# Performance work log

Hardware: AMD Instinct MI355X
Metric: run time of the kernel (lower is better)

Reference implementation:

```python
import jax, jax.numpy as jnp
import numpy as np

N = 50000       # nodes
E = 800000      # edges
IN = 128        # in_channels
HID = 64        # hidden_channels
OUT = 32        # out_channels
H = 4           # heads
EH = 64         # edge_hidden_channels
EOUT = 2        # edge_out_channels
NEG_SLOPE = 0.2 # PyG GATConv default


def gat_conv(x, edge_index, W, att_src, att_dst, bias, num_nodes):
    """PyG GATConv, concat=False, add_self_loops=False, eval mode (no dropout).
    edge_attr is ignored because edge_dim=None (lin_edge is None in PyG).
    Returns (out [N, C], alpha [E, H])."""
    heads, C = att_src.shape
    xl = (x @ W).reshape(-1, heads, C)                 # [N, H, C]
    src, dst = edge_index[0], edge_index[1]
    a_src = jnp.sum(xl * att_src, axis=-1)             # [N, H]
    a_dst = jnp.sum(xl * att_dst, axis=-1)             # [N, H]
    alpha = jax.nn.leaky_relu(a_src[src] + a_dst[dst], NEG_SLOPE)  # [E, H]
    # segment softmax over destination nodes
    amax = jax.ops.segment_max(alpha, dst, num_segments=num_nodes)
    amax = jnp.where(jnp.isfinite(amax), amax, 0.0)
    ex = jnp.exp(alpha - amax[dst])
    denom = jax.ops.segment_sum(ex, dst, num_segments=num_nodes)
    alpha_n = ex / (denom[dst] + 1e-16)                # [E, H]
    msg = xl[src] * alpha_n[:, :, None]                # [E, H, C]
    out = jax.ops.segment_sum(msg, dst, num_segments=num_nodes)  # [N, H, C]
    out = out.mean(axis=1) + bias                      # concat=False -> head mean
    return out, alpha_n


def setup_inputs() -> dict:
    key = jax.random.key(0)
    ks = jax.random.split(key, 16)
    x = jax.random.normal(ks[0], (N, IN), dtype=jnp.float32)
    edge_index = jax.random.randint(ks[1], (2, E), 0, N, dtype=jnp.int32)
    edge_attr = jax.random.normal(ks[2], (E, 5), dtype=jnp.float32)
    s = lambda fan: 1.0 / np.sqrt(fan)
    W1 = jax.random.normal(ks[3], (IN, H * HID), dtype=jnp.float32) * s(IN)
    att1_src = jax.random.normal(ks[4], (H, HID), dtype=jnp.float32) * s(HID)
    att1_dst = jax.random.normal(ks[5], (H, HID), dtype=jnp.float32) * s(HID)
    b1 = jnp.zeros((HID,), dtype=jnp.float32)
    W3 = jax.random.normal(ks[6], (HID, H * OUT), dtype=jnp.float32) * s(HID)
    att3_src = jax.random.normal(ks[7], (H, OUT), dtype=jnp.float32) * s(OUT)
    att3_dst = jax.random.normal(ks[8], (H, OUT), dtype=jnp.float32) * s(OUT)
    b3 = jnp.zeros((OUT,), dtype=jnp.float32)
    EIN = 2 * OUT + H  # cat(out_src, alpha, out_dst)
    mW1 = jax.random.normal(ks[9], (EIN, EH), dtype=jnp.float32) * s(EIN)
    mb1 = jnp.zeros((EH,), dtype=jnp.float32)
    mW2 = jax.random.normal(ks[10], (EH, EOUT), dtype=jnp.float32) * s(EH)
    mb2 = jnp.zeros((EOUT,), dtype=jnp.float32)
    return {"x": x, "edge_index": edge_index, "edge_attr": edge_attr,
            "return_attention_weights": 1,
            "W1": W1, "att1_src": att1_src, "att1_dst": att1_dst, "b1": b1,
            "W3": W3, "att3_src": att3_src, "att3_dst": att3_dst, "b3": b3,
            "mW1": mW1, "mb1": mb1, "mW2": mW2, "mb2": mb2}


def reference(x, edge_index, edge_attr, return_attention_weights,
              W1, att1_src, att1_dst, b1, W3, att3_src, att3_dst, b3,
              mW1, mb1, mW2, mb2):
    edge_len = edge_attr.shape[0]  # == E (no self loops added)
    out, alpha = gat_conv(x, edge_index, W1, att1_src, att1_dst, b1, N)
    out, alpha = gat_conv(out, edge_index, W3, att3_src, att3_dst, b3, N)
    # F.dropout with training=False is the identity (eval mode)
    ei = edge_index[:, :edge_len]
    al = alpha[:edge_len, :]
    out_src = out[ei[0]]                                # [E, OUT]
    out_dst = out[ei[1]]                                # [E, OUT]
    edge_feat = jnp.concatenate([out_src, al, out_dst], axis=-1)  # [E, 2*OUT+H]
    h = jax.nn.relu(edge_feat @ mW1 + mb1)
    edge_out = h @ mW2 + mb2                            # [E, EOUT]
    return (out, edge_out)
```

## Files before the change

### kernel.cpp

```cpp
#include <hip/hip_runtime.h>
#include <hip/hip_fp16.h>

constexpr int NN   = 50000;
constexpr int EE   = 800000;
constexpr int INF  = 128;
constexpr int NH   = 4;
constexpr int GR64 = (NN + 63) / 64;
constexpr int EB   = (EE + 255) / 256;
constexpr int NCH  = (NN + 255) / 256;

struct __align__(8) h4 { __half2 a, b; };

typedef short bf16x8 __attribute__((ext_vector_type(8)));
typedef float f32x4v __attribute__((ext_vector_type(4)));

__device__ __forceinline__ float elw(float a) {
    a = (a > 0.f) ? a : 0.2f * a;
    return __expf(a);
}

__device__ __forceinline__ short bf16_hi(float x) {
    return (short)(__float_as_uint(x) >> 16);
}
__device__ __forceinline__ float bf16_back(short h) {
    return __uint_as_float(((unsigned)(unsigned short)h) << 16);
}

__global__ __launch_bounds__(256) void gemm1_mfma_k(const float* __restrict__ A,
                                                    const float* __restrict__ B,
                                                    __half* __restrict__ C,
                                                    const float* __restrict__ att_s,
                                                    const float* __restrict__ att_d,
                                                    float* __restrict__ a_s,
                                                    float* __restrict__ a_d) {
    __shared__ short Ah[64][72], Al[64][72];
    __shared__ short Bh[64][72], Bl[64][72];
    const int tid  = threadIdx.x;
    const int lane = tid & 63, w = tid >> 6;
    const int row0 = blockIdx.x * 64;
    const int head = blockIdx.y;
    const int c0   = head * 64;

    const int rl = lane & 15, gq = lane >> 4;

    f32x4v acc0 = {0,0,0,0}, acc1 = {0,0,0,0}, acc2 = {0,0,0,0}, acc3 = {0,0,0,0};

    for (int ks = 0; ks < 2; ++ks) {
        {
            const int ar = tid >> 2;
            const int kb = (tid & 3) * 4;
            const int grow = row0 + ar;
            #pragma unroll
            for (int pass = 0; pass < 4; ++pass) {
                const int kl = kb + pass * 16;
                float4 v = make_float4(0.f, 0.f, 0.f, 0.f);
                if (grow < NN) v = *(const float4*)(A + (size_t)grow * 128 + ks * 64 + kl);
                short4 hi, lo;
                hi.x = bf16_hi(v.x); lo.x = bf16_hi(v.x - bf16_back(hi.x));
                hi.y = bf16_hi(v.y); lo.y = bf16_hi(v.y - bf16_back(hi.y));
                hi.z = bf16_hi(v.z); lo.z = bf16_hi(v.z - bf16_back(hi.z));
                hi.w = bf16_hi(v.w); lo.w = bf16_hi(v.w - bf16_back(hi.w));
                *(short4*)&Ah[ar][kl] = hi;
                *(short4*)&Al[ar][kl] = lo;
            }
        }
        {
            const int c  = lane;
            const int kb = w * 16;
            #pragma unroll
            for (int chunk = 0; chunk < 2; ++chunk) {
                short hi8[8], lo8[8];
                #pragma unroll
                for (int i = 0; i < 8; ++i) {
                    const int kl = kb + chunk * 8 + i;
                    const float v = B[(size_t)(ks * 64 + kl) * 256 + c0 + c];
                    hi8[i] = bf16_hi(v);
                    lo8[i] = bf16_hi(v - bf16_back(hi8[i]));
                }
                *(bf16x8*)&Bh[c][kb + chunk * 8] =
                    (bf16x8){hi8[0],hi8[1],hi8[2],hi8[3],hi8[4],hi8[5],hi8[6],hi8[7]};
                *(bf16x8*)&Bl[c][kb + chunk * 8] =
                    (bf16x8){lo8[0],lo8[1],lo8[2],lo8[3],lo8[4],lo8[5],lo8[6],lo8[7]};
            }
        }
        __syncthreads();

        bf16x8 aH0 = *(const bf16x8*)&Ah[w * 16 + rl][gq * 8];
        bf16x8 aH1 = *(const bf16x8*)&Ah[w * 16 + rl][32 + gq * 8];
        bf16x8 aL0 = *(const bf16x8*)&Al[w * 16 + rl][gq * 8];
        bf16x8 aL1 = *(const bf16x8*)&Al[w * 16 + rl][32 + gq * 8];

        #pragma unroll
        for (int cf = 0; cf < 4; ++cf) {
            const int bc = cf * 16 + rl;
            bf16x8 bH0 = *(const bf16x8*)&Bh[bc][gq * 8];
            bf16x8 bH1 = *(const bf16x8*)&Bh[bc][32 + gq * 8];
            bf16x8 bL0 = *(const bf16x8*)&Bl[bc][gq * 8];
            bf16x8 bL1 = *(const bf16x8*)&Bl[bc][32 + gq * 8];
            f32x4v t = (cf == 0) ? acc0 : (cf == 1) ? acc1 : (cf == 2) ? acc2 : acc3;
            t = __builtin_amdgcn_mfma_f32_16x16x32_bf16(aH0, bH0, t, 0, 0, 0);
            t = __builtin_amdgcn_mfma_f32_16x16x32_bf16(aL0, bH0, t, 0, 0, 0);
            t = __builtin_amdgcn_mfma_f32_16x16x32_bf16(aH0, bL0, t, 0, 0, 0);
            t = __builtin_amdgcn_mfma_f32_16x16x32_bf16(aH1, bH1, t, 0, 0, 0);
            t = __builtin_amdgcn_mfma_f32_16x16x32_bf16(aL1, bH1, t, 0, 0, 0);
            t = __builtin_amdgcn_mfma_f32_16x16x32_bf16(aH1, bL1, t, 0, 0, 0);
            if (cf == 0) acc0 = t; else if (cf == 1) acc1 = t;
            else if (cf == 2) acc2 = t; else acc3 = t;
        }
        __syncthreads();
    }

    float sS[4] = {0.f, 0.f, 0.f, 0.f};
    float sD[4] = {0.f, 0.f, 0.f, 0.f};
    #pragma unroll
    for (int cf = 0; cf < 4; ++cf) {
        const f32x4v t = (cf == 0) ? acc0 : (cf == 1) ? acc1 : (cf == 2) ? acc2 : acc3;
        const int gcol = c0 + cf * 16 + rl;
        const float atS = att_s[gcol];
        const float atD = att_d[gcol];
        #pragma unroll
        for (int r = 0; r < 4; ++r) {
            const int grow = row0 + w * 16 + gq * 4 + r;
            if (grow < NN) C[(size_t)grow * 256 + gcol] = __float2half_rn(t[r]);
            sS[r] = fmaf(t[r], atS, sS[r]);
            sD[r] = fmaf(t[r], atD, sD[r]);
        }
    }
    #pragma unroll
    for (int r = 0; r < 4; ++r) {
        #pragma unroll
        for (int msk = 1; msk < 16; msk <<= 1) {
            sS[r] += __shfl_xor(sS[r], msk, 64);
            sD[r] += __shfl_xor(sD[r], msk, 64);
        }
    }
    if (rl == 0) {
        #pragma unroll
        for (int r = 0; r < 4; ++r) {
            const int grow = row0 + w * 16 + gq * 4 + r;
            if (grow < NN) {
                a_s[grow * NH + head] = sS[r];
                a_d[grow * NH + head] = sD[r];
            }
        }
    }
}

__global__ __launch_bounds__(256) void gemm2_mfma_k(const float* __restrict__ A,
                                                    const float* __restrict__ B,
                                                    __half* __restrict__ C,
                                                    const float* __restrict__ att_s,
                                                    const float* __restrict__ att_d,
                                                    float* __restrict__ a_s,
                                                    float* __restrict__ a_d) {
    __shared__ short Ah[64][72], Al[64][72];
    __shared__ short Bh[64][72], Bl[64][72];
    const int tid  = threadIdx.x;
    const int lane = tid & 63, w = tid >> 6;
    const int row0 = blockIdx.x * 64;
    const int c0   = blockIdx.y * 64;
    const int rl = lane & 15, gq = lane >> 4;

    {
        const int ar = tid >> 2;
        const int kb = (tid & 3) * 4;
        const int grow = row0 + ar;
        #pragma unroll
        for (int pass = 0; pass < 4; ++pass) {
            const int kl = kb + pass * 16;
            float4 v = make_float4(0.f, 0.f, 0.f, 0.f);
            if (grow < NN) v = *(const float4*)(A + (size_t)grow * 64 + kl);
            short4 hi, lo;
            hi.x = bf16_hi(v.x); lo.x = bf16_hi(v.x - bf16_back(hi.x));
            hi.y = bf16_hi(v.y); lo.y = bf16_hi(v.y - bf16_back(hi.y));
            hi.z = bf16_hi(v.z); lo.z = bf16_hi(v.z - bf16_back(hi.z));
            hi.w = bf16_hi(v.w); lo.w = bf16_hi(v.w - bf16_back(hi.w));
            *(short4*)&Ah[ar][kl] = hi;
            *(short4*)&Al[ar][kl] = lo;
        }
    }
    {
        const int c  = lane;
        const int kb = w * 16;
        #pragma unroll
        for (int chunk = 0; chunk < 2; ++chunk) {
            short hi8[8], lo8[8];
            #pragma unroll
            for (int i = 0; i < 8; ++i) {
                const int kl = kb + chunk * 8 + i;
                const float v = B[(size_t)kl * 128 + c0 + c];
                hi8[i] = bf16_hi(v);
                lo8[i] = bf16_hi(v - bf16_back(hi8[i]));
            }
            *(bf16x8*)&Bh[c][kb + chunk * 8] =
                (bf16x8){hi8[0],hi8[1],hi8[2],hi8[3],hi8[4],hi8[5],hi8[6],hi8[7]};
            *(bf16x8*)&Bl[c][kb + chunk * 8] =
                (bf16x8){lo8[0],lo8[1],lo8[2],lo8[3],lo8[4],lo8[5],lo8[6],lo8[7]};
        }
    }
    __syncthreads();

    bf16x8 aH0 = *(const bf16x8*)&Ah[w * 16 + rl][gq * 8];
    bf16x8 aH1 = *(const bf16x8*)&Ah[w * 16 + rl][32 + gq * 8];
    bf16x8 aL0 = *(const bf16x8*)&Al[w * 16 + rl][gq * 8];
    bf16x8 aL1 = *(const bf16x8*)&Al[w * 16 + rl][32 + gq * 8];

    f32x4v acc0 = {0,0,0,0}, acc1 = {0,0,0,0}, acc2 = {0,0,0,0}, acc3 = {0,0,0,0};
    #pragma unroll
    for (int cf = 0; cf < 4; ++cf) {
        const int bc = cf * 16 + rl;
        bf16x8 bH0 = *(const bf16x8*)&Bh[bc][gq * 8];
        bf16x8 bH1 = *(const bf16x8*)&Bh[bc][32 + gq * 8];
        bf16x8 bL0 = *(const bf16x8*)&Bl[bc][gq * 8];
        bf16x8 bL1 = *(const bf16x8*)&Bl[bc][32 + gq * 8];
        f32x4v t = (cf == 0) ? acc0 : (cf == 1) ? acc1 : (cf == 2) ? acc2 : acc3;
        t = __builtin_amdgcn_mfma_f32_16x16x32_bf16(aH0, bH0, t, 0, 0, 0);
        t = __builtin_amdgcn_mfma_f32_16x16x32_bf16(aL0, bH0, t, 0, 0, 0);
        t = __builtin_amdgcn_mfma_f32_16x16x32_bf16(aH0, bL0, t, 0, 0, 0);
        t = __builtin_amdgcn_mfma_f32_16x16x32_bf16(aH1, bH1, t, 0, 0, 0);
        t = __builtin_amdgcn_mfma_f32_16x16x32_bf16(aL1, bH1, t, 0, 0, 0);
        t = __builtin_amdgcn_mfma_f32_16x16x32_bf16(aH1, bL1, t, 0, 0, 0);
        if (cf == 0) acc0 = t; else if (cf == 1) acc1 = t;
        else if (cf == 2) acc2 = t; else acc3 = t;
    }

    const int h0 = c0 >> 5, h1 = h0 + 1;
    float sS0[4] = {0,0,0,0}, sD0[4] = {0,0,0,0};
    float sS1[4] = {0,0,0,0}, sD1[4] = {0,0,0,0};
    #pragma unroll
    for (int cf = 0; cf < 4; ++cf) {
        const f32x4v t = (cf == 0) ? acc0 : (cf == 1) ? acc1 : (cf == 2) ? acc2 : acc3;
        const int gcol = c0 + cf * 16 + rl;
        const float atS = att_s[gcol];
        const float atD = att_d[gcol];
        #pragma unroll
        for (int r = 0; r < 4; ++r) {
            const int grow = row0 + w * 16 + gq * 4 + r;
            if (grow < NN) C[(size_t)grow * 128 + gcol] = __float2half_rn(t[r]);
            if (cf < 2) { sS0[r] = fmaf(t[r], atS, sS0[r]); sD0[r] = fmaf(t[r], atD, sD0[r]); }
            else        { sS1[r] = fmaf(t[r], atS, sS1[r]); sD1[r] = fmaf(t[r], atD, sD1[r]); }
        }
    }
    #pragma unroll
    for (int r = 0; r < 4; ++r) {
        #pragma unroll
        for (int msk = 1; msk < 16; msk <<= 1) {
            sS0[r] += __shfl_xor(sS0[r], msk, 64);
            sD0[r] += __shfl_xor(sD0[r], msk, 64);
            sS1[r] += __shfl_xor(sS1[r], msk, 64);
            sD1[r] += __shfl_xor(sD1[r], msk, 64);
        }
    }
    if (rl == 0) {
        #pragma unroll
        for (int r = 0; r < 4; ++r) {
            const int grow = row0 + w * 16 + gq * 4 + r;
            if (grow < NN) {
                a_s[grow * NH + h0] = sS0[r];
                a_d[grow * NH + h0] = sD0[r];
                a_s[grow * NH + h1] = sS1[r];
                a_d[grow * NH + h1] = sD1[r];
            }
        }
    }
}

__global__ __launch_bounds__(256) void gemmpq_mfma_k(const float* __restrict__ A,
                                                     const float* __restrict__ B,
                                                     __half* __restrict__ C) {
    __shared__ short Ah[64][40], Al[64][40];
    __shared__ short Bh[64][40], Bl[64][40];
    const int tid  = threadIdx.x;
    const int lane = tid & 63, w = tid >> 6;
    const int row0 = blockIdx.x * 64;
    const int c0   = blockIdx.y * 64;
    const int rl = lane & 15, gq = lane >> 4;

    {
        const int ar = tid >> 2;
        const int kb = (tid & 3) * 4;
        const int grow = row0 + ar;
        #pragma unroll
        for (int pass = 0; pass < 2; ++pass) {
            const int kl = kb + pass * 16;
            float4 v = make_float4(0.f, 0.f, 0.f, 0.f);
            if (grow < NN) v = *(const float4*)(A + (size_t)grow * 32 + kl);
            short4 hi, lo;
            hi.x = bf16_hi(v.x); lo.x = bf16_hi(v.x - bf16_back(hi.x));
            hi.y = bf16_hi(v.y); lo.y = bf16_hi(v.y - bf16_back(hi.y));
            hi.z = bf16_hi(v.z); lo.z = bf16_hi(v.z - bf16_back(hi.z));
            hi.w = bf16_hi(v.w); lo.w = bf16_hi(v.w - bf16_back(hi.w));
            *(short4*)&Ah[ar][kl] = hi;
            *(short4*)&Al[ar][kl] = lo;
        }
    }
    {
        const int c = lane;
        short hi8[8], lo8[8];
        #pragma unroll
        for (int i = 0; i < 8; ++i) {
            const int kl = w * 8 + i;
            const float v = B[(size_t)kl * 128 + c0 + c];
            hi8[i] = bf16_hi(v);
            lo8[i] = bf16_hi(v - bf16_back(hi8[i]));
        }
        *(bf16x8*)&Bh[c][w * 8] =
            (bf16x8){hi8[0],hi8[1],hi8[2],hi8[3],hi8[4],hi8[5],hi8[6],hi8[7]};
        *(bf16x8*)&Bl[c][w * 8] =
            (bf16x8){lo8[0],lo8[1],lo8[2],lo8[3],lo8[4],lo8[5],lo8[6],lo8[7]};
    }
    __syncthreads();

    bf16x8 aH = *(const bf16x8*)&Ah[w * 16 + rl][gq * 8];
    bf16x8 aL = *(const bf16x8*)&Al[w * 16 + rl][gq * 8];

    #pragma unroll
    for (int cf = 0; cf < 4; ++cf) {
        const int bc = cf * 16 + rl;
        bf16x8 bH = *(const bf16x8*)&Bh[bc][gq * 8];
        bf16x8 bL = *(const bf16x8*)&Bl[bc][gq * 8];
        f32x4v t = {0, 0, 0, 0};
        t = __builtin_amdgcn_mfma_f32_16x16x32_bf16(aH, bH, t, 0, 0, 0);
        t = __builtin_amdgcn_mfma_f32_16x16x32_bf16(aL, bH, t, 0, 0, 0);
        t = __builtin_amdgcn_mfma_f32_16x16x32_bf16(aH, bL, t, 0, 0, 0);
        const int gcol = c0 + cf * 16 + rl;
        #pragma unroll
        for (int r = 0; r < 4; ++r) {
            const int grow = row0 + w * 16 + gq * 4 + r;
            if (grow < NN) C[(size_t)grow * 128 + gcol] = __float2half_rn(t[r]);
        }
    }
}


__device__ __forceinline__ void softagg1_node(int n, int lane,
                                              const int* __restrict__ rowptr,
                                              const int* __restrict__ psrc,
                                              const float* __restrict__ a_s,
                                              const float* __restrict__ a_d,
                                              const __half* __restrict__ xl,
                                              const float* __restrict__ bias,
                                              float* __restrict__ out) {
    const int r0 = rowptr[n], r1 = rowptr[n + 1];
    const int hh = lane >> 4;
    const float ad = a_d[n * NH + hh];

    const h4* X = (const h4*)xl;
    float4 A0 = {0,0,0,0}, A1 = {0,0,0,0}, A2 = {0,0,0,0}, A3 = {0,0,0,0};
    float sum = 0.f;
    int j = r0;
    for (; j + 7 < r1; j += 8) {
        const int s0 = psrc[j],     s1 = psrc[j + 1], s2 = psrc[j + 2], s3 = psrc[j + 3];
        const int s4 = psrc[j + 4], s5 = psrc[j + 5], s6 = psrc[j + 6], s7 = psrc[j + 7];
        const float w0 = elw(a_s[s0 * NH + hh] + ad);
        const float w1 = elw(a_s[s1 * NH + hh] + ad);
        const float w2 = elw(a_s[s2 * NH + hh] + ad);
        const float w3 = elw(a_s[s3 * NH + hh] + ad);
        const float w4 = elw(a_s[s4 * NH + hh] + ad);
        const float w5 = elw(a_s[s5 * NH + hh] + ad);
        const float w6 = elw(a_s[s6 * NH + hh] + ad);
        const float w7 = elw(a_s[s7 * NH + hh] + ad);
        sum += ((w0 + w1) + (w2 + w3)) + ((w4 + w5) + (w6 + w7));
        const h4 v0 = X[(size_t)s0 * 64 + lane];
        const h4 v1 = X[(size_t)s1 * 64 + lane];
        const h4 v2 = X[(size_t)s2 * 64 + lane];
        const h4 v3 = X[(size_t)s3 * 64 + lane];
        const h4 v4 = X[(size_t)s4 * 64 + lane];
        const h4 v5 = X[(size_t)s5 * 64 + lane];
        const h4 v6 = X[(size_t)s6 * 64 + lane];
        const h4 v7 = X[(size_t)s7 * 64 + lane];
        float2 l0 = __half22float2(v0.a), m0 = __half22float2(v0.b);
        float2 l1 = __half22float2(v1.a), m1 = __half22float2(v1.b);
        float2 l2 = __half22float2(v2.a), m2 = __half22float2(v2.b);
        float2 l3 = __half22float2(v3.a), m3 = __half22float2(v3.b);
        float2 l4 = __half22float2(v4.a), m4 = __half22float2(v4.b);
        float2 l5 = __half22float2(v5.a), m5 = __half22float2(v5.b);
        float2 l6 = __half22float2(v6.a), m6 = __half22float2(v6.b);
        float2 l7 = __half22float2(v7.a), m7 = __half22float2(v7.b);
        A0.x = fmaf(w0, l0.x, A0.x); A0.y = fmaf(w0, l0.y, A0.y);
        A0.z = fmaf(w0, m0.x, A0.z); A0.w = fmaf(w0, m0.y, A0.w);
        A1.x = fmaf(w1, l1.x, A1.x); A1.y = fmaf(w1, l1.y, A1.y);
        A1.z = fmaf(w1, m1.x, A1.z); A1.w = fmaf(w1, m1.y, A1.w);
        A2.x = fmaf(w2, l2.x, A2.x); A2.y = fmaf(w2, l2.y, A2.y);
        A2.z = fmaf(w2, m2.x, A2.z); A2.w = fmaf(w2, m2.y, A2.w);
        A3.x = fmaf(w3, l3.x, A3.x); A3.y = fmaf(w3, l3.y, A3.y);
        A3.z = fmaf(w3, m3.x, A3.z); A3.w = fmaf(w3, m3.y, A3.w);
        A0.x = fmaf(w4, l4.x, A0.x); A0.y = fmaf(w4, l4.y, A0.y);
        A0.z = fmaf(w4, m4.x, A0.z); A0.w = fmaf(w4, m4.y, A0.w);
        A1.x = fmaf(w5, l5.x, A1.x); A1.y = fmaf(w5, l5.y, A1.y);
        A1.z = fmaf(w5, m5.x, A1.z); A1.w = fmaf(w5, m5.y, A1.w);
        A2.x = fmaf(w6, l6.x, A2.x); A2.y = fmaf(w6, l6.y, A2.y);
        A2.z = fmaf(w6, m6.x, A2.z); A2.w = fmaf(w6, m6.y, A2.w);
        A3.x = fmaf(w7, l7.x, A3.x); A3.y = fmaf(w7, l7.y, A3.y);
        A3.z = fmaf(w7, m7.x, A3.z); A3.w = fmaf(w7, m7.y, A3.w);
    }
    for (; j < r1; ++j) {
        const int s0 = psrc[j];
        const float w0 = elw(a_s[s0 * NH + hh] + ad);
        sum += w0;
        const h4 v0 = X[(size_t)s0 * 64 + lane];
        float2 l0 = __half22float2(v0.a), m0 = __half22float2(v0.b);
        A0.x = fmaf(w0, l0.x, A0.x); A0.y = fmaf(w0, l0.y, A0.y);
        A0.z = fmaf(w0, m0.x, A0.z); A0.w = fmaf(w0, m0.y, A0.w);
    }
    const float inv = 1.f / (sum + 1e-30f);
    float4 t;
    t.x = ((A0.x + A1.x) + (A2.x + A3.x)) * inv;
    t.y = ((A0.y + A1.y) + (A2.y + A3.y)) * inv;
    t.z = ((A0.z + A1.z) + (A2.z + A3.z)) * inv;
    t.w = ((A0.w + A1.w) + (A2.w + A3.w)) * inv;
    #pragma unroll
    for (int msk = 16; msk < 64; msk <<= 1) {
        t.x += __shfl_xor(t.x, msk, 64);
        t.y += __shfl_xor(t.y, msk, 64);
        t.z += __shfl_xor(t.z, msk, 64);
        t.w += __shfl_xor(t.w, msk, 64);
    }
    if (lane < 16) {
        const float4 b = ((const float4*)bias)[lane];
        float4 o;
        o.x = t.x * 0.25f + b.x; o.y = t.y * 0.25f + b.y;
        o.z = t.z * 0.25f + b.z; o.w = t.w * 0.25f + b.w;
        ((float4*)out)[(size_t)n * 16 + lane] = o;
    }
}

__device__ __forceinline__ void softagg2_node(int n, int lane,
                                              const int* __restrict__ rowptr,
                                              const int* __restrict__ psrc,
                                              const float* __restrict__ a_s,
                                              const float* __restrict__ a_d,
                                              float* __restrict__ alpha_p,
                                              float* __restrict__ inv_s,
                                              const __half* __restrict__ xl,
                                              const float* __restrict__ bias,
                                              float* __restrict__ out) {
    const int r0 = rowptr[n], r1 = rowptr[n + 1];
    const int cl = lane & 31, half = lane >> 5, hh = cl >> 3;
    const float ad = a_d[n * NH + hh];
    const bool writer = (cl & 7) == 0;

    const h4* X = (const h4*)xl;
    float4 A0 = {0,0,0,0}, A1 = {0,0,0,0};
    float sum = 0.f;
    int j = r0;
    for (; j + 7 < r1; j += 8) {
        const int ja = j + half, jc = j + 2 + half, je = j + 4 + half, jg = j + 6 + half;
        const int sa = psrc[ja], sc = psrc[jc], se = psrc[je], sg = psrc[jg];
        const float wa = elw(a_s[sa * NH + hh] + ad);
        const float wc = elw(a_s[sc * NH + hh] + ad);
        const float we = elw(a_s[se * NH + hh] + ad);
        const float wg = elw(a_s[sg * NH + hh] + ad);
        if (writer) {
            alpha_p[ja * NH + hh] = wa; alpha_p[jc * NH + hh] = wc;
            alpha_p[je * NH + hh] = we; alpha_p[jg * NH + hh] = wg;
        }
        sum += (wa + wc) + (we + wg);
        const h4 va = X[(size_t)sa * 32 + cl];
        const h4 vc = X[(size_t)sc * 32 + cl];
        const h4 ve = X[(size_t)se * 32 + cl];
        const h4 vg = X[(size_t)sg * 32 + cl];
        const float2 la = __half22float2(va.a), ma = __half22float2(va.b);
        const float2 lc = __half22float2(vc.a), mc = __half22float2(vc.b);
        const float2 le = __half22float2(ve.a), me = __half22float2(ve.b);
        const float2 lg = __half22float2(vg.a), mg = __half22float2(vg.b);
        A0.x = fmaf(wa, la.x, A0.x); A0.y = fmaf(wa, la.y, A0.y);
        A0.z = fmaf(wa, ma.x, A0.z); A0.w = fmaf(wa, ma.y, A0.w);
        A1.x = fmaf(wc, lc.x, A1.x); A1.y = fmaf(wc, lc.y, A1.y);
        A1.z = fmaf(wc, mc.x, A1.z); A1.w = fmaf(wc, mc.y, A1.w);
        A0.x = fmaf(we, le.x, A0.x); A0.y = fmaf(we, le.y, A0.y);
        A0.z = fmaf(we, me.x, A0.z); A0.w = fmaf(we, me.y, A0.w);
        A1.x = fmaf(wg, lg.x, A1.x); A1.y = fmaf(wg, lg.y, A1.y);
        A1.z = fmaf(wg, mg.x, A1.z); A1.w = fmaf(wg, mg.y, A1.w);
    }
    for (; j < r1; j += 2) {
        const int ja = j + half;
        const bool valid = ja < r1;
        const int sa = psrc[valid ? ja : r0];
        float wa = 0.f;
        if (valid) {
            wa = elw(a_s[sa * NH + hh] + ad);
            if (writer) alpha_p[ja * NH + hh] = wa;
        }
        sum += wa;
        const h4 va = X[(size_t)sa * 32 + cl];
        const float2 la = __half22float2(va.a), ma = __half22float2(va.b);
        A0.x = fmaf(wa, la.x, A0.x); A0.y = fmaf(wa, la.y, A0.y);
        A0.z = fmaf(wa, ma.x, A0.z); A0.w = fmaf(wa, ma.y, A0.w);
    }
    sum += __shfl_xor(sum, 32, 64);
    const float inv = 1.f / (sum + 1e-30f);
    if (writer && half == 0) inv_s[n * NH + hh] = inv;

    float4 t;
    t.x = A0.x + A1.x; t.y = A0.y + A1.y; t.z = A0.z + A1.z; t.w = A0.w + A1.w;
    t.x += __shfl_xor(t.x, 32, 64);
    t.y += __shfl_xor(t.y, 32, 64);
    t.z += __shfl_xor(t.z, 32, 64);
    t.w += __shfl_xor(t.w, 32, 64);
    t.x *= inv; t.y *= inv; t.z *= inv; t.w *= inv;
    #pragma unroll
    for (int q = 0; q < 2; ++q) {
        const int msk = (q == 0) ? 8 : 16;
        t.x += __shfl_xor(t.x, msk, 64);
        t.y += __shfl_xor(t.y, msk, 64);
        t.z += __shfl_xor(t.z, msk, 64);
        t.w += __shfl_xor(t.w, msk, 64);
    }
    if (lane < 8) {
        const float4 b = ((const float4*)bias)[lane];
        float4 o;
        o.x = t.x * 0.25f + b.x; o.y = t.y * 0.25f + b.y;
        o.z = t.z * 0.25f + b.z; o.w = t.w * 0.25f + b.w;
        ((float4*)out)[(size_t)n * 8 + lane] = o;
    }
}


__global__ __launch_bounds__(256) void count_deg_k(const int* __restrict__ ei,
                                                   int* __restrict__ deg) {
    const int e = blockIdx.x * 256 + threadIdx.x;
    if (e < EE) atomicAdd(&deg[ei[EE + e]], 1);
}

__global__ __launch_bounds__(256) void pack_w1_k(const float* __restrict__ mW1,
                                                 float* __restrict__ W1pq) {
    const int idx = blockIdx.x * 256 + threadIdx.x;
    if (idx >= 32 * 128) return;
    const int k = idx >> 7, j = idx & 127;
    W1pq[idx] = (j < 64) ? mW1[k * 64 + j] : mW1[(36 + k) * 64 + (j - 64)];
}

__global__ __launch_bounds__(256) void scan1_k(const int* __restrict__ deg,
                                               int* __restrict__ bsum) {
    __shared__ int sw[4];
    const int tid = threadIdx.x, lane = tid & 63, wv = tid >> 6;
    const int i = blockIdx.x * 256 + tid;
    int s = (i < NN) ? deg[i] : 0;
    #pragma unroll
    for (int d = 1; d < 64; d <<= 1) s += __shfl_xor(s, d, 64);
    if (lane == 0) sw[wv] = s;
    __syncthreads();
    if (tid == 0) bsum[blockIdx.x] = sw[0] + sw[1] + sw[2] + sw[3];
}

__global__ __launch_bounds__(256) void scan2_k(const int* __restrict__ bsum,
                                               int* __restrict__ boff) {
    __shared__ int sw[8];
    const int tid = threadIdx.x, lane = tid & 63, wv = tid >> 6;
    int v = (tid < NCH) ? bsum[tid] : 0;
    int incl = v;
    #pragma unroll
    for (int d = 1; d < 64; d <<= 1) {
        int t = __shfl_up(incl, d, 64);
        if (lane >= d) incl += t;
    }
    if (lane == 63) sw[wv] = incl;
    __syncthreads();
    if (wv == 0 && lane < 4) {
        int s4 = sw[lane];
        #pragma unroll
        for (int d = 1; d < 4; d <<= 1) {
            int t = __shfl_up(s4, d, 64);
            if (lane >= d) s4 += t;
        }
        sw[lane + 4] = s4;
    }
    __syncthreads();
    const int woff = (wv > 0) ? sw[wv - 1 + 4] : 0;
    if (tid < NCH) boff[tid] = woff + incl - v;
}

__global__ __launch_bounds__(256) void scan3_k(const int* __restrict__ deg,
                                               const int* __restrict__ boff,
                                               int* __restrict__ rowptr,
                                               int* __restrict__ cursor) {
    __shared__ int sw[8];
    const int tid = threadIdx.x, lane = tid & 63, wv = tid >> 6;
    const int c = blockIdx.x;
    const int i = c * 256 + tid;
    int v = (i < NN) ? deg[i] : 0;
    int incl = v;
    #pragma unroll
    for (int d = 1; d < 64; d <<= 1) {
        int t = __shfl_up(incl, d, 64);
        if (lane >= d) incl += t;
    }
    if (lane == 63) sw[wv] = incl;
    __syncthreads();
    if (wv == 0 && lane < 4) {
        int s4 = sw[lane];
        #pragma unroll
        for (int d = 1; d < 4; d <<= 1) {
            int t = __shfl_up(s4, d, 64);
            if (lane >= d) s4 += t;
        }
        sw[lane + 4] = s4;
    }
    __syncthreads();
    const int excl = boff[c] + ((wv > 0) ? sw[wv - 1 + 4] : 0) + incl - v;
    if (i < NN) { rowptr[i] = excl; cursor[i] = excl; }
    if (c == 0 && tid == 0) rowptr[NN] = EE;
}

__global__ __launch_bounds__(256) void scatter_perm_k(const int* __restrict__ ei,
                                                      int* __restrict__ cursor,
                                                      int* __restrict__ perm,
                                                      int* __restrict__ psrc,
                                                      int* __restrict__ pdst) {
    const int e = blockIdx.x * 256 + threadIdx.x;
    if (e >= EE) return;
    const int d = ei[EE + e];
    const int p = atomicAdd(&cursor[d], 1);
    perm[p] = e;
    psrc[p] = ei[e];
    pdst[p] = d;
}

__global__ __launch_bounds__(256) void softagg1h_k(const int* __restrict__ rowptr,
                                                   const int* __restrict__ psrc,
                                                   const float* __restrict__ a_s,
                                                   const float* __restrict__ a_d,
                                                   const __half* __restrict__ xl,
                                                   const float* __restrict__ bias,
                                                   float* __restrict__ out) {
    const int n = blockIdx.x * 4 + (threadIdx.x >> 6);
    if (n >= NN) return;
    softagg1_node(n, threadIdx.x & 63, rowptr, psrc, a_s, a_d, xl, bias, out);
}

__global__ __launch_bounds__(256) void softagg2h_k(const int* __restrict__ rowptr,
                                                   const int* __restrict__ psrc,
                                                   const float* __restrict__ a_s,
                                                   const float* __restrict__ a_d,
                                                   float* __restrict__ alpha_p,
                                                   float* __restrict__ inv_s,
                                                   const __half* __restrict__ xl,
                                                   const float* __restrict__ bias,
                                                   float* __restrict__ out) {
    const int n = blockIdx.x * 4 + (threadIdx.x >> 6);
    if (n >= NN) return;
    softagg2_node(n, threadIdx.x & 63, rowptr, psrc, a_s, a_d, alpha_p, inv_s, xl, bias, out);
}

__global__ __launch_bounds__(256) void edge_mlp_k(const __half* __restrict__ PQ,
                                                  const float* __restrict__ alpha_p,
                                                  const float* __restrict__ inv_s,
                                                  const int* __restrict__ psrc,
                                                  const int* __restrict__ pdst,
                                                  const int* __restrict__ perm,
                                                  const float* __restrict__ mW1,
                                                  const float* __restrict__ mb1,
                                                  const float* __restrict__ mW2,
                                                  const float* __restrict__ mb2,
                                                  float* __restrict__ out) {
    const int lane = threadIdx.x & 63, wvv = threadIdx.x >> 6;
    const int g = lane >> 4, c = lane & 15;

    const float4 wa0 = *(const float4*)&mW1[32 * 64 + c * 4];
    const float4 wa1 = *(const float4*)&mW1[33 * 64 + c * 4];
    const float4 wa2 = *(const float4*)&mW1[34 * 64 + c * 4];
    const float4 wa3 = *(const float4*)&mW1[35 * 64 + c * 4];
    const float4 b1v = *(const float4*)&mb1[c * 4];
    const float4 w2a = *(const float4*)&mW2[c * 8];
    const float4 w2b = *(const float4*)&mW2[c * 8 + 4];
    const float bo0 = mb2[0], bo1 = mb2[1];

    const h4* PQ4 = (const h4*)PQ;
    const int gw = blockIdx.x * 4 + wvv;
    const int stride4 = gridDim.x * 4 * 4;

    for (int jb = gw * 4; jb < EE; jb += stride4) {
        const int j = jb + g;
        const int s = psrc[j];
        const int d = pdst[j];
        const float4 ar = *(const float4*)&alpha_p[(size_t)j * 4];
        const float4 iv = *(const float4*)&inv_s[(size_t)d * 4];
        const float al0 = ar.x * iv.x, al1 = ar.y * iv.y;
        const float al2 = ar.z * iv.z, al3 = ar.w * iv.w;
        const h4 ph = PQ4[(size_t)s * 32 + c];
        const h4 qh = PQ4[(size_t)d * 32 + 16 + c];
        const float2 pl = __half22float2(ph.a), pm = __half22float2(ph.b);
        const float2 ql = __half22float2(qh.a), qm = __half22float2(qh.b);
        float4 h;
        h.x = pl.x + ql.x + b1v.x; h.y = pl.y + ql.y + b1v.y;
        h.z = pm.x + qm.x + b1v.z; h.w = pm.y + qm.y + b1v.w;
        h.x = fmaf(al0, wa0.x, h.x); h.y = fmaf(al0, wa0.y, h.y);
        h.z = fmaf(al0, wa0.z, h.z); h.w = fmaf(al0, wa0.w, h.w);
        h.x = fmaf(al1, wa1.x, h.x); h.y = fmaf(al1, wa1.y, h.y);
        h.z = fmaf(al1, wa1.z, h.z); h.w = fmaf(al1, wa1.w, h.w);
        h.x = fmaf(al2, wa2.x, h.x); h.y = fmaf(al2, wa2.y, h.y);
        h.z = fmaf(al2, wa2.z, h.z); h.w = fmaf(al2, wa2.w, h.w);
        h.x = fmaf(al3, wa3.x, h.x); h.y = fmaf(al3, wa3.y, h.y);
        h.z = fmaf(al3, wa3.z, h.z); h.w = fmaf(al3, wa3.w, h.w);
        h.x = fmaxf(h.x, 0.f); h.y = fmaxf(h.y, 0.f);
        h.z = fmaxf(h.z, 0.f); h.w = fmaxf(h.w, 0.f);

        float v0 = h.x * w2a.x + h.y * w2a.z + h.z * w2b.x + h.w * w2b.z;
        float v1 = h.x * w2a.y + h.y * w2a.w + h.z * w2b.y + h.w * w2b.w;
        #pragma unroll
        for (int msk = 1; msk < 16; msk <<= 1) {
            v0 += __shfl_xor(v0, msk, 64);
            v1 += __shfl_xor(v1, msk, 64);
        }
        if (c == 0)
            *(float2*)&out[(size_t)perm[j] * 2] = make_float2(v0 + bo0, v1 + bo1);
    }
}

extern "C" void kernel_launch(void* const* d_in, const int* in_sizes, int n_in,
                              void* d_out, int out_size, void* d_ws, size_t ws_size,
                              hipStream_t stream) {
    const float* x        = (const float*)d_in[0];
    const int*   ei       = (const int*)d_in[1];
    const float* W1       = (const float*)d_in[4];
    const float* att1_src = (const float*)d_in[5];
    const float* att1_dst = (const float*)d_in[6];
    const float* b1       = (const float*)d_in[7];
    const float* W3       = (const float*)d_in[8];
    const float* att3_src = (const float*)d_in[9];
    const float* att3_dst = (const float*)d_in[10];
    const float* b3       = (const float*)d_in[11];
    const float* mW1      = (const float*)d_in[12];
    const float* mb1      = (const float*)d_in[13];
    const float* mW2      = (const float*)d_in[14];
    const float* mb2      = (const float*)d_in[15];

    float* out_nodes = (float*)d_out;
    float* out_edges = out_nodes + (size_t)NN * 32;

    float* ws = (float*)d_ws;
    __half*   xlh     = (__half*)ws;
    __half*   xl2h    = (__half*)ws;
    __half*   PQh     = (__half*)ws;
    float*    h1      = ws + 12800000;
    float*    alpha_p = ws + 16000000;
    float*    a_s     = ws + 25600000;
    float*    a_d     = ws + 25800000;
    float*    W1pq    = ws + 26000000;
    float*    inv_s   = ws + 26100000;
    int*      bsum    = (int*)(ws + 26300000);
    int*      boff    = (int*)(ws + 26301000);
    int*      deg     = (int*)(ws + 26400000);
    int*      cursor  = (int*)(ws + 26450000);
    int*      rowptr  = (int*)(ws + 26500000);
    int*      perm    = (int*)(ws + 26550008);
    int*      psrc    = (int*)(ws + 27350008);
    int*      pdst    = (int*)(ws + 28150008);

    const int NB4 = (NN + 3) / 4;

    hipMemsetAsync(deg, 0, (size_t)NN * 4, stream);
    count_deg_k<<<EB, 256, 0, stream>>>(ei, deg);
    pack_w1_k<<<16, 256, 0, stream>>>(mW1, W1pq);
    gemm1_mfma_k<<<dim3(GR64, 4), 256, 0, stream>>>(x, W1, xlh, att1_src, att1_dst,
                                                    a_s, a_d);
    scan1_k<<<NCH, 256, 0, stream>>>(deg, bsum);
    scan2_k<<<1, 256, 0, stream>>>(bsum, boff);
    scan3_k<<<NCH, 256, 0, stream>>>(deg, boff, rowptr, cursor);
    scatter_perm_k<<<EB, 256, 0, stream>>>(ei, cursor, perm, psrc, pdst);
    softagg1h_k<<<NB4, 256, 0, stream>>>(rowptr, psrc, a_s, a_d, xlh, b1, h1);
    gemm2_mfma_k<<<dim3(GR64, 2), 256, 0, stream>>>(h1, W3, xl2h, att3_src, att3_dst,
                                                    a_s, a_d);
    softagg2h_k<<<NB4, 256, 0, stream>>>(rowptr, psrc, a_s, a_d, alpha_p, inv_s, xl2h, b3,
                                         out_nodes);
    gemmpq_mfma_k<<<dim3(GR64, 2), 256, 0, stream>>>(out_nodes, W1pq, PQh);
    edge_mlp_k<<<2048, 256, 0, stream>>>(PQh, alpha_p, inv_s, psrc, pdst, perm,
                                         mW1, mb1, mW2, mb2, out_edges);
}
```

Measured before the change: 416.7 us.

## Fuse degree count into gemm1 launch and pack src/dst into int2

The degree-counting atomics now run inside the first GEMM launch: even blocks count degrees and odd blocks do the GEMM tiles, which removes one kernel launch and lets the two independent jobs overlap. Source and destination index arrays are merged into one interleaved int2 array, so the edge MLP loads both with one 8-byte access. The softmax aggregation kernels only need the source index, so they now read strided int2 entries and waste half of each fetch. The block interleave also changes the GEMM tile order and grid size.

```diff
diff --git a/kernel.cpp b/kernel.cpp
--- a/kernel.cpp
+++ b/kernel.cpp
@@ -26,21 +26,34 @@
     return __uint_as_float(((unsigned)(unsigned short)h) << 16);
 }
 
-__global__ __launch_bounds__(256) void gemm1_mfma_k(const float* __restrict__ A,
-                                                    const float* __restrict__ B,
-                                                    __half* __restrict__ C,
-                                                    const float* __restrict__ att_s,
-                                                    const float* __restrict__ att_d,
-                                                    float* __restrict__ a_s,
-                                                    float* __restrict__ a_d) {
+__global__ __launch_bounds__(256) void cnt_gemm1_k(const int* __restrict__ ei,
+                                                   int* __restrict__ deg,
+                                                   const float* __restrict__ A,
+                                                   const float* __restrict__ B,
+                                                   __half* __restrict__ C,
+                                                   const float* __restrict__ att_s,
+                                                   const float* __restrict__ att_d,
+                                                   float* __restrict__ a_s,
+                                                   float* __restrict__ a_d) {
     __shared__ short Ah[64][72], Al[64][72];
     __shared__ short Bh[64][72], Bl[64][72];
-    const int tid  = threadIdx.x;
+    const int b = blockIdx.x;
+    const int tid = threadIdx.x;
+
+    if ((b & 1) == 0) {
+        const int eb = b >> 1;
+        if (eb < EB) {
+            const int e = eb * 256 + tid;
+            if (e < EE) atomicAdd(&deg[ei[EE + e]], 1);
+        }
+        return;
+    }
+
+    const int t    = b >> 1;
     const int lane = tid & 63, w = tid >> 6;
-    const int row0 = blockIdx.x * 64;
-    const int head = blockIdx.y;
+    const int row0 = (t % GR64) * 64;
+    const int head = t / GR64;
     const int c0   = head * 64;
-
     const int rl = lane & 15, gq = lane >> 4;
 
     f32x4v acc0 = {0,0,0,0}, acc1 = {0,0,0,0}, acc2 = {0,0,0,0}, acc3 = {0,0,0,0};
@@ -97,15 +110,15 @@
             bf16x8 bH1 = *(const bf16x8*)&Bh[bc][32 + gq * 8];
             bf16x8 bL0 = *(const bf16x8*)&Bl[bc][gq * 8];
             bf16x8 bL1 = *(const bf16x8*)&Bl[bc][32 + gq * 8];
-            f32x4v t = (cf == 0) ? acc0 : (cf == 1) ? acc1 : (cf == 2) ? acc2 : acc3;
-            t = __builtin_amdgcn_mfma_f32_16x16x32_bf16(aH0, bH0, t, 0, 0, 0);
-            t = __builtin_amdgcn_mfma_f32_16x16x32_bf16(aL0, bH0, t, 0, 0, 0);
-            t = __builtin_amdgcn_mfma_f32_16x16x32_bf16(aH0, bL0, t, 0, 0, 0);
-            t = __builtin_amdgcn_mfma_f32_16x16x32_bf16(aH1, bH1, t, 0, 0, 0);
-            t = __builtin_amdgcn_mfma_f32_16x16x32_bf16(aL1, bH1, t, 0, 0, 0);
-            t = __builtin_amdgcn_mfma_f32_16x16x32_bf16(aH1, bL1, t, 0, 0, 0);
-            if (cf == 0) acc0 = t; else if (cf == 1) acc1 = t;
-            else if (cf == 2) acc2 = t; else acc3 = t;
+            f32x4v tacc = (cf == 0) ? acc0 : (cf == 1) ? acc1 : (cf == 2) ? acc2 : acc3;
+            tacc = __builtin_amdgcn_mfma_f32_16x16x32_bf16(aH0, bH0, tacc, 0, 0, 0);
+            tacc = __builtin_amdgcn_mfma_f32_16x16x32_bf16(aL0, bH0, tacc, 0, 0, 0);
+            tacc = __builtin_amdgcn_mfma_f32_16x16x32_bf16(aH0, bL0, tacc, 0, 0, 0);
+            tacc = __builtin_amdgcn_mfma_f32_16x16x32_bf16(aH1, bH1, tacc, 0, 0, 0);
+            tacc = __builtin_amdgcn_mfma_f32_16x16x32_bf16(aL1, bH1, tacc, 0, 0, 0);
+            tacc = __builtin_amdgcn_mfma_f32_16x16x32_bf16(aH1, bL1, tacc, 0, 0, 0);
+            if (cf == 0) acc0 = tacc; else if (cf == 1) acc1 = tacc;
+            else if (cf == 2) acc2 = tacc; else acc3 = tacc;
         }
         __syncthreads();
     }
@@ -114,16 +127,16 @@
     float sD[4] = {0.f, 0.f, 0.f, 0.f};
     #pragma unroll
     for (int cf = 0; cf < 4; ++cf) {
-        const f32x4v t = (cf == 0) ? acc0 : (cf == 1) ? acc1 : (cf == 2) ? acc2 : acc3;
+        const f32x4v tacc = (cf == 0) ? acc0 : (cf == 1) ? acc1 : (cf == 2) ? acc2 : acc3;
         const int gcol = c0 + cf * 16 + rl;
         const float atS = att_s[gcol];
         const float atD = att_d[gcol];
         #pragma unroll
         for (int r = 0; r < 4; ++r) {
             const int grow = row0 + w * 16 + gq * 4 + r;
-            if (grow < NN) C[(size_t)grow * 256 + gcol] = __float2half_rn(t[r]);
-            sS[r] = fmaf(t[r], atS, sS[r]);
-            sD[r] = fmaf(t[r], atD, sD[r]);
+            if (grow < NN) C[(size_t)grow * 256 + gcol] = __float2half_rn(tacc[r]);
+            sS[r] = fmaf(tacc[r], atS, sS[r]);
+            sD[r] = fmaf(tacc[r], atD, sD[r]);
         }
     }
     #pragma unroll
@@ -335,7 +348,7 @@
 
 __device__ __forceinline__ void softagg1_node(int n, int lane,
                                               const int* __restrict__ rowptr,
-                                              const int* __restrict__ psrc,
+                                              const int2* __restrict__ psd,
                                               const float* __restrict__ a_s,
                                               const float* __restrict__ a_d,
                                               const __half* __restrict__ xl,
@@ -350,8 +363,8 @@
     float sum = 0.f;
     int j = r0;
     for (; j + 7 < r1; j += 8) {
-        const int s0 = psrc[j],     s1 = psrc[j + 1], s2 = psrc[j + 2], s3 = psrc[j + 3];
-        const int s4 = psrc[j + 4], s5 = psrc[j + 5], s6 = psrc[j + 6], s7 = psrc[j + 7];
+        const int s0 = psd[j].x,     s1 = psd[j + 1].x, s2 = psd[j + 2].x, s3 = psd[j + 3].x;
+        const int s4 = psd[j + 4].x, s5 = psd[j + 5].x, s6 = psd[j + 6].x, s7 = psd[j + 7].x;
         const float w0 = elw(a_s[s0 * NH + hh] + ad);
         const float w1 = elw(a_s[s1 * NH + hh] + ad);
         const float w2 = elw(a_s[s2 * NH + hh] + ad);
@@ -395,7 +408,7 @@
         A3.z = fmaf(w7, m7.x, A3.z); A3.w = fmaf(w7, m7.y, A3.w);
     }
     for (; j < r1; ++j) {
-        const int s0 = psrc[j];
+        const int s0 = psd[j].x;
         const float w0 = elw(a_s[s0 * NH + hh] + ad);
         sum += w0;
         const h4 v0 = X[(size_t)s0 * 64 + lane];
@@ -427,7 +440,7 @@
 
 __device__ __forceinline__ void softagg2_node(int n, int lane,
                                               const int* __restrict__ rowptr,
-                                              const int* __restrict__ psrc,
+                                              const int2* __restrict__ psd,
                                               const float* __restrict__ a_s,
                                               const float* __restrict__ a_d,
                                               float* __restrict__ alpha_p,
@@ -446,7 +459,7 @@
     int j = r0;
     for (; j + 7 < r1; j += 8) {
         const int ja = j + half, jc = j + 2 + half, je = j + 4 + half, jg = j + 6 + half;
-        const int sa = psrc[ja], sc = psrc[jc], se = psrc[je], sg = psrc[jg];
+        const int sa = psd[ja].x, sc = psd[jc].x, se = psd[je].x, sg = psd[jg].x;
         const float wa = elw(a_s[sa * NH + hh] + ad);
         const float wc = elw(a_s[sc * NH + hh] + ad);
         const float we = elw(a_s[se * NH + hh] + ad);
@@ -476,7 +489,7 @@
     for (; j < r1; j += 2) {
         const int ja = j + half;
         const bool valid = ja < r1;
-        const int sa = psrc[valid ? ja : r0];
+        const int sa = psd[valid ? ja : r0].x;
         float wa = 0.f;
         if (valid) {
             wa = elw(a_s[sa * NH + hh] + ad);
@@ -516,12 +529,6 @@
     }
 }
 
-
-__global__ __launch_bounds__(256) void count_deg_k(const int* __restrict__ ei,
-                                                   int* __restrict__ deg) {
-    const int e = blockIdx.x * 256 + threadIdx.x;
-    if (e < EE) atomicAdd(&deg[ei[EE + e]], 1);
-}
 
 __global__ __launch_bounds__(256) void pack_w1_k(const float* __restrict__ mW1,
                                                  float* __restrict__ W1pq) {
@@ -606,19 +613,18 @@
 __global__ __launch_bounds__(256) void scatter_perm_k(const int* __restrict__ ei,
                                                       int* __restrict__ cursor,
                                                       int* __restrict__ perm,
-                                                      int* __restrict__ psrc,
-                                                      int* __restrict__ pdst) {
+                                                      int2* __restrict__ psd) {
     const int e = blockIdx.x * 256 + threadIdx.x;
     if (e >= EE) return;
-    const int d = ei[EE + e];
-    const int p = atomicAdd(&cursor[d], 1);
+    const int sv = ei[e];
+    const int dv = ei[EE + e];
+    const int p = atomicAdd(&cursor[dv], 1);
     perm[p] = e;
-    psrc[p] = ei[e];
-    pdst[p] = d;
+    psd[p] = make_int2(sv, dv);
 }
 
 __global__ __launch_bounds__(256) void softagg1h_k(const int* __restrict__ rowptr,
-                                                   const int* __restrict__ psrc,
+                                                   const int2* __restrict__ psd,
                                                    const float* __restrict__ a_s,
                                                    const float* __restrict__ a_d,
                                                    const __half* __restrict__ xl,
@@ -626,11 +632,11 @@
                                                    float* __restrict__ out) {
     const int n = blockIdx.x * 4 + (threadIdx.x >> 6);
     if (n >= NN) return;
-    softagg1_node(n, threadIdx.x & 63, rowptr, psrc, a_s, a_d, xl, bias, out);
+    softagg1_node(n, threadIdx.x & 63, rowptr, psd, a_s, a_d, xl, bias, out);
 }
 
 __global__ __launch_bounds__(256) void softagg2h_k(const int* __restrict__ rowptr,
-                                                   const int* __restrict__ psrc,
+                                                   const int2* __restrict__ psd,
                                                    const float* __restrict__ a_s,
                                                    const float* __restrict__ a_d,
                                                    float* __restrict__ alpha_p,
@@ -640,14 +646,13 @@
                                                    float* __restrict__ out) {
     const int n = blockIdx.x * 4 + (threadIdx.x >> 6);
     if (n >= NN) return;
-    softagg2_node(n, threadIdx.x & 63, rowptr, psrc, a_s, a_d, alpha_p, inv_s, xl, bias, out);
+    softagg2_node(n, threadIdx.x & 63, rowptr, psd, a_s, a_d, alpha_p, inv_s, xl, bias, out);
 }
 
 __global__ __launch_bounds__(256) void edge_mlp_k(const __half* __restrict__ PQ,
                                                   const float* __restrict__ alpha_p,
                                                   const float* __restrict__ inv_s,
-                                                  const int* __restrict__ psrc,
-                                                  const int* __restrict__ pdst,
+                                                  const int2* __restrict__ psd,
                                                   const int* __restrict__ perm,
                                                   const float* __restrict__ mW1,
                                                   const float* __restrict__ mb1,
@@ -672,8 +677,9 @@
 
     for (int jb = gw * 4; jb < EE; jb += stride4) {
         const int j = jb + g;
-        const int s = psrc[j];
-        const int d = pdst[j];
+        const int2 sd = psd[j];
+        const int s = sd.x;
+        const int d = sd.y;
         const float4 ar = *(const float4*)&alpha_p[(size_t)j * 4];
         const float4 iv = *(const float4*)&inv_s[(size_t)d * 4];
         const float al0 = ar.x * iv.x, al1 = ar.y * iv.y;
@@ -745,26 +751,24 @@
     int*      cursor  = (int*)(ws + 26450000);
     int*      rowptr  = (int*)(ws + 26500000);
     int*      perm    = (int*)(ws + 26550008);
-    int*      psrc    = (int*)(ws + 27350008);
-    int*      pdst    = (int*)(ws + 28150008);
+    int2*     psd     = (int2*)(ws + 27350008);
 
     const int NB4 = (NN + 3) / 4;
 
     hipMemsetAsync(deg, 0, (size_t)NN * 4, stream);
-    count_deg_k<<<EB, 256, 0, stream>>>(ei, deg);
     pack_w1_k<<<16, 256, 0, stream>>>(mW1, W1pq);
-    gemm1_mfma_k<<<dim3(GR64, 4), 256, 0, stream>>>(x, W1, xlh, att1_src, att1_dst,
-                                                    a_s, a_d);
+    cnt_gemm1_k<<<2 * GR64 * 4, 256, 0, stream>>>(ei, deg, x, W1, xlh,
+                                                  att1_src, att1_dst, a_s, a_d);
     scan1_k<<<NCH, 256, 0, stream>>>(deg, bsum);
     scan2_k<<<1, 256, 0, stream>>>(bsum, boff);
     scan3_k<<<NCH, 256, 0, stream>>>(deg, boff, rowptr, cursor);
-    scatter_perm_k<<<EB, 256, 0, stream>>>(ei, cursor, perm, psrc, pdst);
-    softagg1h_k<<<NB4, 256, 0, stream>>>(rowptr, psrc, a_s, a_d, xlh, b1, h1);
+    scatter_perm_k<<<EB, 256, 0, stream>>>(ei, cursor, perm, psd);
+    softagg1h_k<<<NB4, 256, 0, stream>>>(rowptr, psd, a_s, a_d, xlh, b1, h1);
     gemm2_mfma_k<<<dim3(GR64, 2), 256, 0, stream>>>(h1, W3, xl2h, att3_src, att3_dst,
                                                     a_s, a_d);
-    softagg2h_k<<<NB4, 256, 0, stream>>>(rowptr, psrc, a_s, a_d, alpha_p, inv_s, xl2h, b3,
+    softagg2h_k<<<NB4, 256, 0, stream>>>(rowptr, psd, a_s, a_d, alpha_p, inv_s, xl2h, b3,
                                          out_nodes);
     gemmpq_mfma_k<<<dim3(GR64, 2), 256, 0, stream>>>(out_nodes, W1pq, PQh);
-    edge_mlp_k<<<2048, 256, 0, stream>>>(PQh, alpha_p, inv_s, psrc, pdst, perm,
+    edge_mlp_k<<<2048, 256, 0, stream>>>(PQh, alpha_p, inv_s, psd, perm,
                                          mW1, mb1, mW2, mb2, out_edges);
 }
```

Result: faster. 405.5 us (-2.7%).
